# Kernel tuning notes

Hardware: AMD Instinct MI355X
Metric: run time of the kernel (lower is better)

Reference implementation:

```python
import jax, jax.numpy as jnp
import numpy as np

B, S, IN, H, L = 512, 1024, 64, 32, 4


def setup_inputs() -> dict:
    key = jax.random.key(0)
    ks = jax.random.split(key, 9)
    s = 1.0 / np.sqrt(H)  # PyTorch RNN/Linear init scale
    u = lambda k, shape: jax.random.uniform(k, shape, jnp.float32, -s, s)
    return {
        "x": jax.random.normal(ks[0], (B, S, IN), jnp.float32),
        "h_state": jnp.zeros((L, B, H), jnp.float32),
        "W_ih0": u(ks[1], (H, IN)),          # layer 0 input weights
        "W_ih_rest": u(ks[2], (L - 1, H, H)),  # layers 1..3 input weights
        "W_hh": u(ks[3], (L, H, H)),
        "b_ih": u(ks[4], (L, H)),
        "b_hh": u(ks[5], (L, H)),
        "fc_w": u(ks[6], (1, H)),
        "fc_b": u(ks[7], (1,)),
    }


def _rnn_layer(seq_sbf, h0, W_ih, W_hh, b):
    # seq_sbf: [S, B, F]; vanilla RNN: h_t = tanh(x_t W_ih^T + h_{t-1} W_hh^T + b)
    def step(h, x_t):
        h = jnp.tanh(x_t @ W_ih.T + h @ W_hh.T + b)
        return h, h
    return jax.lax.scan(step, h0, seq_sbf)


def reference(x, h_state, W_ih0, W_ih_rest, W_hh, b_ih, b_hh, fc_w, fc_b):
    seq = jnp.swapaxes(x, 0, 1)  # [S, B, IN]
    h_finals = []
    for l in range(L):  # fixed small layer count
        W_ih = W_ih0 if l == 0 else W_ih_rest[l - 1]
        h_last, seq = _rnn_layer(seq, h_state[l], W_ih, W_hh[l], b_ih[l] + b_hh[l])
        h_finals.append(h_last)
    r_out = jnp.swapaxes(seq, 0, 1)                 # [B, S, H]
    logits = (r_out @ fc_w.T + fc_b)[..., 0]        # fused per-timestep Linear -> [B, S]
    probs = jax.nn.softmax(logits, axis=-1)         # nn.Softmax over last (seq) dim
    return probs, jnp.stack(h_finals, axis=0)       # [B,S], [L,B,H]
```

## Files before the change

kernel.cpp:

```cpp
#include <hip/hip_runtime.h>


#define BB 512
#define SS 1024
#define INF 64
#define HH 32
#define LL 4
#define KB 16

typedef __fp16 v2h __attribute__((ext_vector_type(2)));

__device__ __forceinline__ v2h bch(unsigned u) { return __builtin_bit_cast(v2h, u); }
__device__ __forceinline__ unsigned bcu(v2h h) { return __builtin_bit_cast(unsigned, h); }

template <int CTRL>
__device__ __forceinline__ float dpp_add(float v) {
  int y = __builtin_amdgcn_update_dpp(0, __float_as_int(v), CTRL, 0xF, 0xF, true);
  return v + __int_as_float(y);
}
template <int CTRL>
__device__ __forceinline__ float dpp_mov(float v) {
  int y = __builtin_amdgcn_update_dpp(0, __float_as_int(v), CTRL, 0xF, 0xF, true);
  return __int_as_float(y);
}

__device__ __forceinline__ float tanh_fast(float a) {
  const float e = __builtin_amdgcn_exp2f(a * 2.885390081777927f);
  const float r = __builtin_amdgcn_rcpf(e + 1.0f);
  return __builtin_fmaf(-2.0f, r, 1.0f);
}

__device__ __forceinline__ float dot16p(const v2h* w, const v2h* v) {
  float a = 0.f, c = 0.f;
#pragma unroll
  for (int j = 0; j < 4; ++j) {
    a = __builtin_amdgcn_fdot2(w[2 * j + 0], v[2 * j + 0], a, false);
    c = __builtin_amdgcn_fdot2(w[2 * j + 1], v[2 * j + 1], c, false);
  }
  return a + c;
}

#define BAR() asm volatile("s_waitcnt lgkmcnt(0)\n\ts_barrier" ::: "memory")

__global__ __launch_bounds__(256) void u0_kernel(
    const float* __restrict__ x, const float* __restrict__ W_ih0,
    const float* __restrict__ b_ih, const float* __restrict__ b_hh,
    float* __restrict__ u0) {
  __shared__ float Wl[HH * INF];
  __shared__ float bl[HH];
  const int tid = threadIdx.x;
  {
    const float4* src = (const float4*)W_ih0;
    float4* dst = (float4*)Wl;
    dst[tid] = src[tid];
    dst[tid + 256] = src[tid + 256];
    if (tid < HH) bl[tid] = b_ih[tid] + b_hh[tid];
  }
  __syncthreads();

  const int row = blockIdx.x * 256 + tid;
  const float4* xr = (const float4*)(x + (size_t)row * INF);
  float acc[HH];
#pragma unroll
  for (int u = 0; u < HH; ++u) acc[u] = bl[u];
#pragma unroll 4
  for (int kc = 0; kc < 16; ++kc) {
    const float4 xv = xr[kc];
#pragma unroll
    for (int u = 0; u < HH; ++u) {
      const float4 wv = ((const float4*)Wl)[u * 16 + kc];
      acc[u] += wv.x * xv.x + wv.y * xv.y + wv.z * xv.z + wv.w * xv.w;
    }
  }
  float4* op = (float4*)(u0 + (size_t)row * HH);
#pragma unroll
  for (int j = 0; j < 8; ++j)
    op[j] = make_float4(acc[4 * j], acc[4 * j + 1], acc[4 * j + 2], acc[4 * j + 3]);
}

__global__ __launch_bounds__(256, 2) void rnn_kernel(
    const float* __restrict__ u0g_all, const float* __restrict__ h_state,
    const float* __restrict__ W_ih_rest, const float* __restrict__ W_hh,
    const float* __restrict__ b_ih, const float* __restrict__ b_hh,
    const float* __restrict__ fc_w, const float* __restrict__ fc_b,
    float* __restrict__ out) {
  __shared__ int hb[LL][2][KB][16];
  __shared__ float h3f[2][KB][32];
  __shared__ float lrow[SS];
  __shared__ float red[8];

  const int tid  = threadIdx.x;
  const int wid  = tid >> 6;
  const int lane = tid & 63;
  const int b    = blockIdx.x;
  const int ks   = lane & 1;
  const int h    = lane >> 1;

  v2h wih[8], whh[8];
  {
    const float2* ph = (const float2*)(W_hh + (size_t)(wid * HH + h) * HH + ks * 16);
#pragma unroll
    for (int j = 0; j < 8; ++j) whh[j] = __builtin_amdgcn_cvt_pkrtz(ph[j].x, ph[j].y);
  }
  float bias = 0.f;
  if (wid > 0) {
    const float2* pi =
        (const float2*)(W_ih_rest + (size_t)((wid - 1) * HH + h) * HH + ks * 16);
#pragma unroll
    for (int j = 0; j < 8; ++j) wih[j] = __builtin_amdgcn_cvt_pkrtz(pi[j].x, pi[j].y);
    bias = b_ih[wid * HH + h] + b_hh[wid * HH + h];
  }
  const float fcwh = fc_w[h] * 0.5f;
  const float fcb  = fc_b[0];

  v2h sv[8];
  {
    const float2* hs = (const float2*)(h_state + (size_t)(wid * BB + b) * HH);
#pragma unroll
    for (int j = 0; j < 8; ++j)
      sv[j] = __builtin_amdgcn_cvt_pkrtz(hs[ks * 8 + j].x, hs[ks * 8 + j].y);
  }

  const float* ug = u0g_all + (size_t)b * SS * HH;
  float* const hfin = out + (size_t)BB * SS;

  auto ld8 = [&](const int* p, v2h* v) __attribute__((always_inline)) {
    const uint4* q = (const uint4*)p;
    uint4 A = q[0], B = q[1];
    v[0] = bch(A.x); v[1] = bch(A.y); v[2] = bch(A.z); v[3] = bch(A.w);
    v[4] = bch(B.x); v[5] = bch(B.y); v[6] = bch(B.z); v[7] = bch(B.w);
  };
  auto packpair = [&](float hv) __attribute__((always_inline)) {
    return bcu(__builtin_amdgcn_cvt_pkrtz(hv, dpp_mov<0xEE>(hv)));
  };
  auto store_pk = [&](int l, int buf, int slot, unsigned pk) __attribute__((always_inline)) {
    if ((lane & 3) == 0) hb[l][buf][slot][lane >> 2] = (int)pk;
  };
  auto fcred = [&](float v) __attribute__((always_inline)) {
    v = dpp_add<0x111>(v);
    v = dpp_add<0x112>(v);
    v = dpp_add<0x114>(v);
    v = dpp_add<0x118>(v);
    v = dpp_add<0x142>(v);
    v = dpp_add<0x143>(v);
    return v;
  };

  if (wid == 0) {
    float urA[KB], urB[KB];
#pragma unroll
    for (int i = 0; i < KB; ++i) urA[i] = ug[i * HH + h];
    auto iter0 = [&](int n, int buf, float* urC, float* urN)
        __attribute__((always_inline)) {
      BAR();
      const bool fc_on = (n >= 4);
      const bool cw    = (n <= 63);
      float a[KB];
      if (fc_on) {
#pragma unroll
        for (int i = 0; i < KB; ++i) a[i] = h3f[buf ^ 1][i][h];
      }
      if (cw) {
        const int tb = KB * (n + 1);
#pragma unroll
        for (int i = 0; i < KB; ++i) {
          int t = tb + i; t = t < SS ? t : SS - 1;
          urN[i] = ug[t * HH + h];
        }
        float hvL = 0.f;
#pragma unroll
        for (int i = 0; i < KB; ++i) {
          float acc = dot16p(whh, sv);
          acc = dpp_add<0xB1>(acc) + urC[i];
          const float hv = tanh_fast(acc);
          const unsigned pk = packpair(hv);
          store_pk(0, buf, i, pk);
          ld8(&hb[0][buf][i][ks * 8], sv);
          if (i == KB - 1) hvL = hv;
        }
        if (n == 63 && ks == 0) hfin[(0 * BB + b) * HH + h] = hvL;
      }
      if (fc_on) {
        const int tf0 = KB * (n - 4);
#pragma unroll
        for (int i = 0; i < KB; ++i) {
          float v = fcred(a[i] * fcwh);
          if (lane == 63) lrow[tf0 + i] = v + fcb;
        }
      }
    };
    for (int n0 = 0; n0 < 68; n0 += 2) {
      iter0(n0, 0, urA, urB);
      iter0(n0 + 1, 1, urB, urA);
    }
  } else {
    v2h viA[4][8], viB[4][8];
    auto ldgrp = [&](int buf, int g, v2h (*vv)[8]) __attribute__((always_inline)) {
#pragma unroll
      for (int q = 0; q < 4; ++q)
        ld8(&hb[wid - 1][buf ^ 1][g * 4 + q][ks * 8], vv[q]);
    };
    auto dogrp = [&](int n, int buf, int g, v2h (*vc)[8], float& hvL)
        __attribute__((always_inline)) {
#pragma unroll
      for (int q = 0; q < 4; ++q) {
        const int i = g * 4 + q;
        float accA = dot16p(wih, vc[q]);
        float acc = accA + dot16p(whh, sv);
        acc = dpp_add<0xB1>(acc) + bias;
        const float hv = tanh_fast(acc);
        const unsigned pk = packpair(hv);
        store_pk(wid, buf, i, pk);
        if (wid == 3 && ks == 0) h3f[buf][i][h] = hv;
        ld8(&hb[wid][buf][i][ks * 8], sv);
        if (i == KB - 1) hvL = hv;
      }
    };
    auto iterl = [&](int n, int buf) __attribute__((always_inline)) {
      BAR();
      const bool cw = (n >= wid && n <= 63 + wid);
      if (cw) {
        float hvL = 0.f;
        ldgrp(buf, 0, viA);
        ldgrp(buf, 1, viB);
        dogrp(n, buf, 0, viA, hvL);
        ldgrp(buf, 2, viA);
        dogrp(n, buf, 1, viB, hvL);
        ldgrp(buf, 3, viB);
        dogrp(n, buf, 2, viA, hvL);
        dogrp(n, buf, 3, viB, hvL);
        if (n == 63 + wid && ks == 0) hfin[(wid * BB + b) * HH + h] = hvL;
      }
    };
    for (int n0 = 0; n0 < 68; n0 += 2) {
      iterl(n0, 0);
      iterl(n0 + 1, 1);
    }
  }

  __syncthreads();
  {
    float4 v = ((const float4*)lrow)[tid];
    float m = fmaxf(fmaxf(v.x, v.y), fmaxf(v.z, v.w));
#pragma unroll
    for (int d = 32; d >= 1; d >>= 1) m = fmaxf(m, __shfl_xor(m, d));
    if ((tid & 63) == 0) red[tid >> 6] = m;
    __syncthreads();
    m = fmaxf(fmaxf(red[0], red[1]), fmaxf(red[2], red[3]));
    const float e0 = __expf(v.x - m), e1 = __expf(v.y - m);
    const float e2 = __expf(v.z - m), e3 = __expf(v.w - m);
    float s = (e0 + e1) + (e2 + e3);
#pragma unroll
    for (int d = 32; d >= 1; d >>= 1) s += __shfl_xor(s, d);
    if ((tid & 63) == 0) red[4 + (tid >> 6)] = s;
    __syncthreads();
    s = (red[4] + red[5]) + (red[6] + red[7]);
    const float inv = 1.0f / s;
    float4 o;
    o.x = e0 * inv; o.y = e1 * inv; o.z = e2 * inv; o.w = e3 * inv;
    ((float4*)(out + (size_t)b * SS))[tid] = o;
  }
}

extern "C" void kernel_launch(void* const* d_in, const int* in_sizes, int n_in,
                              void* d_out, int out_size, void* d_ws, size_t ws_size,
                              hipStream_t stream) {
  const float* x         = (const float*)d_in[0];
  const float* h_state   = (const float*)d_in[1];
  const float* W_ih0     = (const float*)d_in[2];
  const float* W_ih_rest = (const float*)d_in[3];
  const float* W_hh      = (const float*)d_in[4];
  const float* b_ih      = (const float*)d_in[5];
  const float* b_hh      = (const float*)d_in[6];
  const float* fc_w      = (const float*)d_in[7];
  const float* fc_b      = (const float*)d_in[8];
  float* out = (float*)d_out;
  float* u0  = (float*)d_ws;

  hipLaunchKernelGGL(u0_kernel, dim3((BB * SS) / 256), dim3(256), 0, stream,
                     x, W_ih0, b_ih, b_hh, u0);
  hipLaunchKernelGGL(rnn_kernel, dim3(BB), dim3(256), 0, stream,
                     u0, h_state, W_ih_rest, W_hh, b_ih, b_hh, fc_w, fc_b, out);
}
```

Baseline: 427.5 us.

## Fuse layer-0 input projection into RNN kernel via producer warps

Removes the separate u0 kernel and its global workspace round trip. Four extra warps per block compute the layer-0 input projection for the next time block into double-buffered LDS, while the four recurrent warps consume it, with both sides synchronised by the existing per-block barrier. This drops writing and rereading a B*S*H intermediate and one kernel launch. In exchange the block doubles to 512 threads, which may reduce occupancy, and every barrier now also waits on the producer warps.

```diff
diff --git a/kernel.cpp b/kernel.cpp
--- a/kernel.cpp
+++ b/kernel.cpp
@@ -42,50 +42,15 @@
 
 #define BAR() asm volatile("s_waitcnt lgkmcnt(0)\n\ts_barrier" ::: "memory")
 
-__global__ __launch_bounds__(256) void u0_kernel(
-    const float* __restrict__ x, const float* __restrict__ W_ih0,
-    const float* __restrict__ b_ih, const float* __restrict__ b_hh,
-    float* __restrict__ u0) {
-  __shared__ float Wl[HH * INF];
-  __shared__ float bl[HH];
-  const int tid = threadIdx.x;
-  {
-    const float4* src = (const float4*)W_ih0;
-    float4* dst = (float4*)Wl;
-    dst[tid] = src[tid];
-    dst[tid + 256] = src[tid + 256];
-    if (tid < HH) bl[tid] = b_ih[tid] + b_hh[tid];
-  }
-  __syncthreads();
-
-  const int row = blockIdx.x * 256 + tid;
-  const float4* xr = (const float4*)(x + (size_t)row * INF);
-  float acc[HH];
-#pragma unroll
-  for (int u = 0; u < HH; ++u) acc[u] = bl[u];
-#pragma unroll 4
-  for (int kc = 0; kc < 16; ++kc) {
-    const float4 xv = xr[kc];
-#pragma unroll
-    for (int u = 0; u < HH; ++u) {
-      const float4 wv = ((const float4*)Wl)[u * 16 + kc];
-      acc[u] += wv.x * xv.x + wv.y * xv.y + wv.z * xv.z + wv.w * xv.w;
-    }
-  }
-  float4* op = (float4*)(u0 + (size_t)row * HH);
-#pragma unroll
-  for (int j = 0; j < 8; ++j)
-    op[j] = make_float4(acc[4 * j], acc[4 * j + 1], acc[4 * j + 2], acc[4 * j + 3]);
-}
-
-__global__ __launch_bounds__(256, 2) void rnn_kernel(
-    const float* __restrict__ u0g_all, const float* __restrict__ h_state,
-    const float* __restrict__ W_ih_rest, const float* __restrict__ W_hh,
-    const float* __restrict__ b_ih, const float* __restrict__ b_hh,
-    const float* __restrict__ fc_w, const float* __restrict__ fc_b,
-    float* __restrict__ out) {
+__global__ __launch_bounds__(512, 4) void rnn_kernel(
+    const float* __restrict__ x, const float* __restrict__ h_state,
+    const float* __restrict__ W_ih0, const float* __restrict__ W_ih_rest,
+    const float* __restrict__ W_hh, const float* __restrict__ b_ih,
+    const float* __restrict__ b_hh, const float* __restrict__ fc_w,
+    const float* __restrict__ fc_b, float* __restrict__ out) {
   __shared__ int hb[LL][2][KB][16];
   __shared__ float h3f[2][KB][32];
+  __shared__ float lu0[2][KB][32];
   __shared__ float lrow[SS];
   __shared__ float red[8];
 
@@ -97,31 +62,38 @@
   const int h    = lane >> 1;
 
   v2h wih[8], whh[8];
-  {
+  float bias = 0.f;
+  if (wid < LL) {
     const float2* ph = (const float2*)(W_hh + (size_t)(wid * HH + h) * HH + ks * 16);
 #pragma unroll
     for (int j = 0; j < 8; ++j) whh[j] = __builtin_amdgcn_cvt_pkrtz(ph[j].x, ph[j].y);
-  }
-  float bias = 0.f;
-  if (wid > 0) {
-    const float2* pi =
-        (const float2*)(W_ih_rest + (size_t)((wid - 1) * HH + h) * HH + ks * 16);
-#pragma unroll
-    for (int j = 0; j < 8; ++j) wih[j] = __builtin_amdgcn_cvt_pkrtz(pi[j].x, pi[j].y);
-    bias = b_ih[wid * HH + h] + b_hh[wid * HH + h];
+    if (wid > 0) {
+      const float2* pi =
+          (const float2*)(W_ih_rest + (size_t)((wid - 1) * HH + h) * HH + ks * 16);
+#pragma unroll
+      for (int j = 0; j < 8; ++j) wih[j] = __builtin_amdgcn_cvt_pkrtz(pi[j].x, pi[j].y);
+      bias = b_ih[wid * HH + h] + b_hh[wid * HH + h];
+    }
+  }
+  float4 wv4[8];
+  float bias0 = 0.f;
+  if (wid >= LL) {
+    const float4* wr = (const float4*)(W_ih0 + (size_t)h * INF + ks * 32);
+#pragma unroll
+    for (int j = 0; j < 8; ++j) wv4[j] = wr[j];
+    bias0 = b_ih[h] + b_hh[h];
   }
   const float fcwh = fc_w[h] * 0.5f;
   const float fcb  = fc_b[0];
 
   v2h sv[8];
-  {
+  if (wid < LL) {
     const float2* hs = (const float2*)(h_state + (size_t)(wid * BB + b) * HH);
 #pragma unroll
     for (int j = 0; j < 8; ++j)
       sv[j] = __builtin_amdgcn_cvt_pkrtz(hs[ks * 8 + j].x, hs[ks * 8 + j].y);
   }
 
-  const float* ug = u0g_all + (size_t)b * SS * HH;
   float* const hfin = out + (size_t)BB * SS;
 
   auto ld8 = [&](const int* p, v2h* v) __attribute__((always_inline)) {
@@ -147,12 +119,9 @@
   };
 
   if (wid == 0) {
-    float urA[KB], urB[KB];
-#pragma unroll
-    for (int i = 0; i < KB; ++i) urA[i] = ug[i * HH + h];
-    auto iter0 = [&](int n, int buf, float* urC, float* urN)
-        __attribute__((always_inline)) {
+    for (int n = 0; n < 68; ++n) {
       BAR();
+      const int buf = n & 1;
       const bool fc_on = (n >= 4);
       const bool cw    = (n <= 63);
       float a[KB];
@@ -161,17 +130,14 @@
         for (int i = 0; i < KB; ++i) a[i] = h3f[buf ^ 1][i][h];
       }
       if (cw) {
-        const int tb = KB * (n + 1);
-#pragma unroll
-        for (int i = 0; i < KB; ++i) {
-          int t = tb + i; t = t < SS ? t : SS - 1;
-          urN[i] = ug[t * HH + h];
-        }
+        float ur[KB];
+#pragma unroll
+        for (int i = 0; i < KB; ++i) ur[i] = lu0[buf][i][h];
         float hvL = 0.f;
 #pragma unroll
         for (int i = 0; i < KB; ++i) {
           float acc = dot16p(whh, sv);
-          acc = dpp_add<0xB1>(acc) + urC[i];
+          acc = dpp_add<0xB1>(acc) + ur[i];
           const float hv = tanh_fast(acc);
           const unsigned pk = packpair(hv);
           store_pk(0, buf, i, pk);
@@ -188,12 +154,8 @@
           if (lane == 63) lrow[tf0 + i] = v + fcb;
         }
       }
-    };
-    for (int n0 = 0; n0 < 68; n0 += 2) {
-      iter0(n0, 0, urA, urB);
-      iter0(n0 + 1, 1, urB, urA);
-    }
-  } else {
+    }
+  } else if (wid < LL) {
     v2h viA[4][8], viB[4][8];
     auto ldgrp = [&](int buf, int g, v2h (*vv)[8]) __attribute__((always_inline)) {
 #pragma unroll
@@ -236,24 +198,53 @@
       iterl(n0, 0);
       iterl(n0 + 1, 1);
     }
+  } else {
+    const int p = wid - LL;
+    const float* xb = x + (size_t)b * SS * INF;
+    auto produce = [&](int blk) __attribute__((always_inline)) {
+      const int buf = blk & 1;
+      const int T = KB * blk + 4 * p;
+#pragma unroll
+      for (int q = 0; q < 4; ++q) {
+        const float4* x4 = (const float4*)(xb + (size_t)(T + q) * INF + ks * 32);
+        float acc = 0.f;
+#pragma unroll
+        for (int j = 0; j < 8; ++j) {
+          const float4 xv = x4[j];
+          acc += wv4[j].x * xv.x + wv4[j].y * xv.y + wv4[j].z * xv.z + wv4[j].w * xv.w;
+        }
+        const float tot = dpp_add<0xB1>(acc) + bias0;
+        if (ks == 0) lu0[buf][4 * p + q][h] = tot;
+      }
+    };
+    produce(0);
+    for (int n = 0; n < 68; ++n) {
+      BAR();
+      if (n <= 62) produce(n + 1);
+    }
   }
 
   __syncthreads();
-  {
-    float4 v = ((const float4*)lrow)[tid];
-    float m = fmaxf(fmaxf(v.x, v.y), fmaxf(v.z, v.w));
+  float4 v; float m; float e0, e1, e2, e3; float s;
+  if (tid < 256) {
+    v = ((const float4*)lrow)[tid];
+    m = fmaxf(fmaxf(v.x, v.y), fmaxf(v.z, v.w));
 #pragma unroll
     for (int d = 32; d >= 1; d >>= 1) m = fmaxf(m, __shfl_xor(m, d));
     if ((tid & 63) == 0) red[tid >> 6] = m;
-    __syncthreads();
+  }
+  __syncthreads();
+  if (tid < 256) {
     m = fmaxf(fmaxf(red[0], red[1]), fmaxf(red[2], red[3]));
-    const float e0 = __expf(v.x - m), e1 = __expf(v.y - m);
-    const float e2 = __expf(v.z - m), e3 = __expf(v.w - m);
-    float s = (e0 + e1) + (e2 + e3);
+    e0 = __expf(v.x - m); e1 = __expf(v.y - m);
+    e2 = __expf(v.z - m); e3 = __expf(v.w - m);
+    s = (e0 + e1) + (e2 + e3);
 #pragma unroll
     for (int d = 32; d >= 1; d >>= 1) s += __shfl_xor(s, d);
     if ((tid & 63) == 0) red[4 + (tid >> 6)] = s;
-    __syncthreads();
+  }
+  __syncthreads();
+  if (tid < 256) {
     s = (red[4] + red[5]) + (red[6] + red[7]);
     const float inv = 1.0f / s;
     float4 o;
@@ -275,10 +266,8 @@
   const float* fc_w      = (const float*)d_in[7];
   const float* fc_b      = (const float*)d_in[8];
   float* out = (float*)d_out;
-  float* u0  = (float*)d_ws;
-
-  hipLaunchKernelGGL(u0_kernel, dim3((BB * SS) / 256), dim3(256), 0, stream,
-                     x, W_ih0, b_ih, b_hh, u0);
-  hipLaunchKernelGGL(rnn_kernel, dim3(BB), dim3(256), 0, stream,
-                     u0, h_state, W_ih_rest, W_hh, b_ih, b_hh, fc_w, fc_b, out);
-}
+
+  hipLaunchKernelGGL(rnn_kernel, dim3(BB), dim3(512), 0, stream,
+                     x, h_state, W_ih0, W_ih_rest, W_hh, b_ih, b_hh,
+                     fc_w, fc_b, out);
+}
```

New measurement: 411.1 us. 3.8% less time.
